# Performance work log

Hardware: AMD Instinct MI355X
Metric: run time of the kernel (lower is better)

Reference implementation:

```python
import jax, jax.numpy as jnp
import numpy as np

C = 512
CI = C // 4  # inter_channels
EPS = 1e-5


def _conv1x1(x, w, b):
    # x: [B,C,H,W], w: [O,C], b: [O] -> [B,O,H,W]
    return jnp.einsum('bchw,oc->bohw', x, w) + b[None, :, None, None]


def _maxpool2(t):
    # 2x2 max pool, stride 2 (NCHW)
    b, c, h, w = t.shape
    return t.reshape(b, c, h // 2, 2, w // 2, 2).max(axis=(3, 5))


def setup_inputs() -> dict:
    key = jax.random.key(0)
    ks = jax.random.split(key, 9)
    B, H, W = 8, 64, 64
    s_in = 1.0 / np.sqrt(C)
    s_ci = 1.0 / np.sqrt(CI)
    return {
        'x': jax.random.normal(ks[0], (B, C, H, W), jnp.float32),
        'g_w': jax.random.normal(ks[1], (CI, C), jnp.float32) * s_in,
        'g_b': jnp.zeros((CI,), jnp.float32),
        'phi_w': jax.random.normal(ks[2], (CI, C), jnp.float32) * s_in,
        'phi_b': jnp.zeros((CI,), jnp.float32),
        'theta_w': jax.random.normal(ks[3], (CI, C), jnp.float32) * s_in,
        'theta_b': jnp.zeros((CI,), jnp.float32),
        'W_w': jax.random.normal(ks[4], (C, CI), jnp.float32) * s_ci,
        'W_b': jnp.zeros((C,), jnp.float32),
        'ln_gamma': jax.random.normal(ks[5], (C,), jnp.float32) * 0.02 + 1.0,
        'ln_beta': jnp.zeros((C,), jnp.float32),
    }


def reference(x, g_w, g_b, phi_w, phi_b, theta_w, theta_b, W_w, W_b, ln_gamma, ln_beta):
    B, Cc, H, Wd = x.shape
    N = H * Wd
    # projections; g and phi are maxpool-downsampled (N/4 key/value positions)
    g_x = _maxpool2(_conv1x1(x, g_w, g_b)).reshape(B, CI, N // 4)          # [B,Ci,M]
    phi_x = _maxpool2(_conv1x1(x, phi_w, phi_b)).reshape(B, CI, N // 4)    # [B,Ci,M]
    theta_x = _conv1x1(x, theta_w, theta_b).reshape(B, CI, N)              # [B,Ci,N]
    # attention: QK^T -> softmax -> V
    f = jnp.einsum('bcn,bcm->bnm', theta_x, phi_x)                          # [B,N,M]
    attn = jax.nn.softmax(f, axis=-1)
    y = jnp.einsum('bnm,bcm->bcn', attn, g_x).reshape(B, CI, H, Wd)         # [B,Ci,H,W]
    # output projection + channels-first LayerNorm + residual
    W_y = _conv1x1(y, W_w, W_b)                                             # [B,C,H,W]
    mu = W_y.mean(axis=1, keepdims=True)
    var = W_y.var(axis=1, keepdims=True)
    W_y = (W_y - mu) * jax.lax.rsqrt(var + EPS)
    W_y = W_y * ln_gamma[None, :, None, None] + ln_beta[None, :, None, None]
    return W_y + x
```

## Files before the change

### kernel.cpp

```cpp
#include <hip/hip_runtime.h>
#include <math.h>

constexpr int Cc  = 512;
constexpr int CIc = 128;
constexpr int Bc  = 8;
constexpr int Nc  = 4096;
constexpr int Mc  = 1024;

typedef __bf16 bf16x8 __attribute__((ext_vector_type(8)));
typedef float  f32x4  __attribute__((ext_vector_type(4)));

__device__ __forceinline__ unsigned short f2bf(float f) {
  unsigned u = __float_as_uint(f);
  u += 0x7fffu + ((u >> 16) & 1u);
  return (unsigned short)(u >> 16);
}
__device__ __forceinline__ float bf2f(unsigned short h) {
  return __uint_as_float((unsigned)h << 16);
}
__device__ __forceinline__ unsigned pack2bf(float lo, float hi) {
  return (unsigned)f2bf(lo) | ((unsigned)f2bf(hi) << 16);
}

__device__ __forceinline__ void gload16(const void* g, void* lds) {
  __builtin_amdgcn_global_load_lds(
      (const __attribute__((address_space(1))) unsigned int*)g,
      (__attribute__((address_space(3))) unsigned int*)lds, 16, 0, 0);
}

__global__ __launch_bounds__(256) void k_prep(
    const float* __restrict__ gw, const float* __restrict__ pw,
    const float* __restrict__ tw, const float* __restrict__ Ww,
    const float* __restrict__ gb, const float* __restrict__ pb,
    const float* __restrict__ tb,
    unsigned short* __restrict__ wcat, unsigned short* __restrict__ wwb,
    float* __restrict__ bcat) {
  constexpr float L2E = 1.4426950408889634f;
  int i = blockIdx.x * 256 + threadIdx.x;
  if (i < 49152) {
    int c = i >> 7, q = i & 127;
    const float* src = (c < 128) ? tw + (size_t)c * 512
                     : (c < 256) ? pw + (size_t)(c - 128) * 512
                                 : gw + (size_t)(c - 256) * 512;
    float sc = (c < 128) ? L2E : 1.f;
    float4 v = *(const float4*)(src + q * 4);
    ushort4 o;
    o.x = f2bf(v.x * sc); o.y = f2bf(v.y * sc);
    o.z = f2bf(v.z * sc); o.w = f2bf(v.w * sc);
    *(ushort4*)(wcat + (size_t)c * 512 + q * 4) = o;
  } else if (i < 65536) {
    int i2 = i - 49152;
    int c = i2 >> 5, q = i2 & 31;
    float4 v = *(const float4*)(Ww + (size_t)c * 128 + q * 4);
    ushort4 o;
    o.x = f2bf(v.x); o.y = f2bf(v.y); o.z = f2bf(v.z); o.w = f2bf(v.w);
    *(ushort4*)(wwb + (size_t)c * 128 + q * 4) = o;
  } else if (i < 65920) {
    int j = i - 65536;
    bcat[j] = (j < 128) ? tb[j] * L2E : (j < 256) ? pb[j - 128] : gb[j - 256];
  }
}

__global__ __launch_bounds__(512) void k_conv_all(
    const float* __restrict__ x, const unsigned short* __restrict__ wcat,
    const float* __restrict__ bcat,
    unsigned short* __restrict__ theta_t, unsigned short* __restrict__ phi_t,
    unsigned short* __restrict__ gbuf) {
  __shared__ __align__(16) char smem[147456];
  const int b = blockIdx.y, h2 = blockIdx.x, n0 = h2 * 128;
  const int t = threadIdx.x;
  const int w = t >> 6, l = t & 63, lr = l & 15, lg = l >> 4;

  const char* wsrc = (const char*)wcat;
  int woff[6];
#pragma unroll
  for (int i = 0; i < 6; ++i) {
    int r = (w * 6 + i) * 8 + (l >> 3);
    woff[i] = r * 1024 + (((l & 7) * 16) ^ ((r & 7) << 4));
  }

  const float* xb = x + (size_t)b * Cc * Nc + n0 + w * 16 + lr;

  float xraw0[16], xraw1[16];
#define LOADX(dst_, k0_)                                                  \
  {                                                                       \
    _Pragma("unroll")                                                     \
    for (int ks = 0; ks < 2; ++ks)                                        \
      _Pragma("unroll")                                                   \
      for (int j = 0; j < 8; ++j)                                         \
        dst_[ks * 8 + j] = xb[(size_t)((k0_) + ks * 32 + lg * 8 + j) * Nc]; \
  }
#define STAGEW(buf_, k0_)                                                 \
  {                                                                       \
    char* dst_ = smem + (buf_) * 49152;                                   \
    _Pragma("unroll")                                                     \
    for (int i = 0; i < 6; ++i)                                           \
      gload16(wsrc + (size_t)(k0_) * 2 + woff[i], dst_ + (w * 6 + i) * 1024); \
  }
#define CONVERT(src_)                                                     \
  {                                                                       \
    _Pragma("unroll")                                                     \
    for (int ks = 0; ks < 2; ++ks) {                                      \
      union { unsigned u[4]; bf16x8 v; } ab;                              \
      _Pragma("unroll")                                                   \
      for (int q = 0; q < 4; ++q)                                         \
        ab.u[q] = pack2bf(src_[ks * 8 + 2 * q], src_[ks * 8 + 2 * q + 1]); \
      af[ks] = ab.v;                                                      \
    }                                                                     \
  }

  f32x4 acc[24];
#pragma unroll
  for (int tc = 0; tc < 24; ++tc) acc[tc] = (f32x4){0.f, 0.f, 0.f, 0.f};

  STAGEW(0, 0);
  LOADX(xraw0, 0);
  STAGEW(1, 64);
  LOADX(xraw1, 64);
  asm volatile("s_waitcnt vmcnt(22)" ::: "memory");
  __builtin_amdgcn_s_barrier();

#pragma unroll
  for (int c = 0; c < 8; ++c) {
    bf16x8 af[2];
    if ((c & 1) == 0) {
      CONVERT(xraw0);
      if (c < 6) { STAGEW((c + 2) % 3, (c + 2) * 64); LOADX(xraw0, (c + 2) * 64); }
    } else {
      CONVERT(xraw1);
      if (c < 6) { STAGEW((c + 2) % 3, (c + 2) * 64); LOADX(xraw1, (c + 2) * 64); }
    }
    const char* Wb = smem + (c % 3) * 49152;
    __builtin_amdgcn_s_setprio(1);
#pragma unroll
    for (int ks = 0; ks < 2; ++ks)
#pragma unroll
      for (int tc = 0; tc < 24; ++tc) {
        int r = tc * 16 + lr;
        bf16x8 bfr = *(const bf16x8*)(
            Wb + r * 128 + ((lg * 16 + ks * 64) ^ ((lr & 7) << 4)));
        acc[tc] = __builtin_amdgcn_mfma_f32_16x16x32_bf16(af[ks], bfr, acc[tc], 0, 0, 0);
      }
    __builtin_amdgcn_s_setprio(0);
    if (c < 6) {
      asm volatile("s_waitcnt vmcnt(22)" ::: "memory");
      __builtin_amdgcn_s_barrier();
    } else if (c == 6) {
      asm volatile("s_waitcnt vmcnt(16)" ::: "memory");
      __builtin_amdgcn_s_barrier();
    }
  }
#undef LOADX
#undef STAGEW
#undef CONVERT

  __syncthreads();
  unsigned short* PG = (unsigned short*)smem;
  unsigned short* Yt = (unsigned short*)(smem + 67584);
  const int rbase = w * 16 + lg * 4;

#pragma unroll
  for (int tc = 8; tc < 24; ++tc) {
    float bv = bcat[tc * 16 + lr];
#pragma unroll
    for (int reg = 0; reg < 4; ++reg)
      PG[(rbase + reg) * 264 + tc * 16 + lr - 128] = f2bf(acc[tc][reg] + bv);
  }
  if (w < 4) {
#pragma unroll
    for (int tc = 0; tc < 8; ++tc) {
      float bv = bcat[tc * 16 + lr];
#pragma unroll
      for (int reg = 0; reg < 4; ++reg)
        Yt[(rbase + reg) * 136 + tc * 16 + lr] = f2bf(acc[tc][reg] + bv);
    }
  }
  __syncthreads();
#pragma unroll
  for (int it = 0; it < 2; ++it) {
    int idx = it * 512 + t, n = idx >> 4, j = idx & 15;
    *(bf16x8*)(theta_t + (((size_t)(b * Nc + n0 + n)) << 7) + j * 8) =
        *(const bf16x8*)(Yt + n * 136 + j * 8);
  }
  {
    int mloc = t >> 4, j = t & 15;
    const unsigned short* r0 = &PG[(2 * mloc) * 264 + j * 8];
    const unsigned short* r1 = &PG[(2 * mloc + 1) * 264 + j * 8];
    const unsigned short* r2 = &PG[(64 + 2 * mloc) * 264 + j * 8];
    const unsigned short* r3 = &PG[(65 + 2 * mloc) * 264 + j * 8];
    unsigned short o[8];
#pragma unroll
    for (int q = 0; q < 8; ++q)
      o[q] = f2bf(fmaxf(fmaxf(bf2f(r0[q]), bf2f(r1[q])),
                        fmaxf(bf2f(r2[q]), bf2f(r3[q]))));
    unsigned short* dp = phi_t + (((size_t)(b * Mc + h2 * 32 + mloc)) << 7) + j * 8;
    *(ushort4*)dp = *(ushort4*)o;
    *(ushort4*)(dp + 4) = *(ushort4*)(o + 4);
  }
  {
    int ci = t >> 2, mq = t & 3;
    unsigned short tmp[8];
#pragma unroll
    for (int q = 0; q < 8; ++q) {
      int w2 = mq * 8 + q;
      float m0 = fmaxf(
          fmaxf(bf2f(PG[(2 * w2) * 264 + 128 + ci]),
                bf2f(PG[(2 * w2 + 1) * 264 + 128 + ci])),
          fmaxf(bf2f(PG[(64 + 2 * w2) * 264 + 128 + ci]),
                bf2f(PG[(65 + 2 * w2) * 264 + 128 + ci])));
      tmp[q] = f2bf(m0);
    }
    unsigned short* dst = gbuf + ((size_t)(b * CIc + ci)) * Mc + h2 * 32 + mq * 8;
    *(ushort4*)(dst) = *(ushort4*)(tmp);
    *(ushort4*)(dst + 4) = *(ushort4*)(tmp + 4);
  }
  __syncthreads();
  if (w >= 4) {
#pragma unroll
    for (int tc = 0; tc < 8; ++tc) {
      float bv = bcat[tc * 16 + lr];
#pragma unroll
      for (int reg = 0; reg < 4; ++reg)
        Yt[((w - 4) * 16 + lg * 4 + reg) * 136 + tc * 16 + lr] =
            f2bf(acc[tc][reg] + bv);
    }
  }
  __syncthreads();
#pragma unroll
  for (int it = 0; it < 2; ++it) {
    int idx = it * 512 + t, n = idx >> 4, j = idx & 15;
    *(bf16x8*)(theta_t + (((size_t)(b * Nc + n0 + 64 + n)) << 7) + j * 8) =
        *(const bf16x8*)(Yt + n * 136 + j * 8);
  }
}

__global__ __launch_bounds__(256) void k_attn_mfma(
    const unsigned short* __restrict__ theta_t,
    const unsigned short* __restrict__ phi_t,
    const unsigned short* __restrict__ gv,
    unsigned short* __restrict__ y_t) {
  __shared__ __align__(16) char Kb[2][16384];
  __shared__ __align__(16) char Vb[2][16384];
  __shared__ __align__(16) unsigned Psd[4][16][36];
  const int b = blockIdx.y, n0 = blockIdx.x * 64;
  const int tid = threadIdx.x;
  const int w = tid >> 6, l = tid & 63;
  const int lr = l & 15, lg = l >> 4;

  const int krow_l = l >> 4, kchunk = (l & 15) * 16;
  const int vrow_l = l >> 3, vchunk = (l & 7) * 16;
  int koff[4], voff[4];
#pragma unroll
  for (int i = 0; i < 4; ++i) {
    int kr = w * 16 + i * 4 + krow_l;
    koff[i] = kr * 256 + (kchunk ^ ((kr & 7) << 4));
    int vr = w * 32 + i * 8 + vrow_l;
    voff[i] = vr * 2048 + (vchunk ^ ((vr & 7) << 4));
  }
  const char* kbase = (const char*)(phi_t + (((size_t)(b * Mc)) << 7));
  const char* vbase = (const char*)(gv + (((size_t)b) << 17));

  auto stage = [&](int buf, int t) {
#pragma unroll
    for (int i = 0; i < 4; ++i)
      gload16(kbase + t * 16384 + koff[i], &Kb[buf][(w * 4 + i) * 1024]);
#pragma unroll
    for (int i = 0; i < 4; ++i)
      gload16(vbase + t * 128 + voff[i], &Vb[buf][(w * 4 + i) * 1024]);
  };

  bf16x8 qf[4];
  {
    const unsigned short* qp =
        theta_t + (((size_t)(b * Nc + n0 + w * 16 + lr)) << 7);
#pragma unroll
    for (int kk = 0; kk < 4; ++kk)
      qf[kk] = *(const bf16x8*)(qp + kk * 32 + lg * 8);
  }
  f32x4 of[8];
#pragma unroll
  for (int ct = 0; ct < 8; ++ct) of[ct] = (f32x4){0.f, 0.f, 0.f, 0.f};
  float run_m = -1e30f, run_l = 0.f;

  stage(0, 0);
  asm volatile("s_waitcnt vmcnt(0)" ::: "memory");
  __builtin_amdgcn_s_barrier();

  for (int t = 0; t < Mc / 64; ++t) {
    const int cur = t & 1;
    if (t + 1 < Mc / 64) stage(cur ^ 1, t + 1);
    const char* Ks = Kb[cur];
    const char* Vs = Vb[cur];
    f32x4 sm[4];
    __builtin_amdgcn_s_setprio(1);
#pragma unroll
    for (int mt = 0; mt < 4; ++mt) {
      f32x4 s = (f32x4){0.f, 0.f, 0.f, 0.f};
#pragma unroll
      for (int kk = 0; kk < 4; ++kk) {
        bf16x8 kf = *(const bf16x8*)(
            Ks + (mt * 16 + lr) * 256 + ((kk * 64 + lg * 16) ^ ((lr & 7) << 4)));
        s = __builtin_amdgcn_mfma_f32_16x16x32_bf16(kf, qf[kk], s, 0, 0, 0);
      }
      sm[mt] = s;
    }
    __builtin_amdgcn_s_setprio(0);
    float mx;
    {
      float m0 = fmaxf(fmaxf(sm[0][0], sm[0][1]), fmaxf(sm[0][2], sm[0][3]));
      float m1 = fmaxf(fmaxf(sm[1][0], sm[1][1]), fmaxf(sm[1][2], sm[1][3]));
      float m2 = fmaxf(fmaxf(sm[2][0], sm[2][1]), fmaxf(sm[2][2], sm[2][3]));
      float m3 = fmaxf(fmaxf(sm[3][0], sm[3][1]), fmaxf(sm[3][2], sm[3][3]));
      mx = fmaxf(fmaxf(m0, m1), fmaxf(m2, m3));
      mx = fmaxf(mx, __shfl_xor(mx, 16));
      mx = fmaxf(mx, __shfl_xor(mx, 32));
    }
    if (__any(mx > run_m + 8.f)) {
      float nm = fmaxf(run_m, mx);
      float sc = __builtin_amdgcn_exp2f(run_m - nm);
      run_m = nm;
      run_l *= sc;
#pragma unroll
      for (int reg = 0; reg < 4; ++reg) {
        float scr = __shfl(sc, lg * 20 + reg);
#pragma unroll
        for (int ct = 0; ct < 8; ++ct) of[ct][reg] *= scr;
      }
    }
    unsigned pk[4][2];
    float rowsum = 0.f;
#pragma unroll
    for (int mt = 0; mt < 4; ++mt) {
      float p0 = __builtin_amdgcn_exp2f(sm[mt][0] - run_m);
      float p1 = __builtin_amdgcn_exp2f(sm[mt][1] - run_m);
      float p2 = __builtin_amdgcn_exp2f(sm[mt][2] - run_m);
      float p3 = __builtin_amdgcn_exp2f(sm[mt][3] - run_m);
      rowsum += (p0 + p1) + (p2 + p3);
      asm("v_cvt_pk_bf16_f32 %0, %1, %2" : "=v"(pk[mt][0]) : "v"(p0), "v"(p1));
      asm("v_cvt_pk_bf16_f32 %0, %1, %2" : "=v"(pk[mt][1]) : "v"(p2), "v"(p3));
    }
    rowsum += __shfl_xor(rowsum, 16);
    rowsum += __shfl_xor(rowsum, 32);
    run_l += rowsum;
#pragma unroll
    for (int mt = 0; mt < 4; ++mt) {
      Psd[w][lr][8 * mt + 2 * lg + 0] = pk[mt][0];
      Psd[w][lr][8 * mt + 2 * lg + 1] = pk[mt][1];
    }
    bf16x8 pa0 = *(const bf16x8*)&Psd[w][lr][lg * 4];
    bf16x8 pa1 = *(const bf16x8*)&Psd[w][lr][16 + lg * 4];
    __builtin_amdgcn_s_setprio(1);
#pragma unroll
    for (int ct = 0; ct < 8; ++ct) {
      bf16x8 vf0 = *(const bf16x8*)(
          Vs + (ct * 16 + lr) * 128 + ((lg * 16) ^ ((lr & 7) << 4)));
      of[ct] = __builtin_amdgcn_mfma_f32_16x16x32_bf16(pa0, vf0, of[ct], 0, 0, 0);
      bf16x8 vf1 = *(const bf16x8*)(
          Vs + (ct * 16 + lr) * 128 + ((64 + lg * 16) ^ ((lr & 7) << 4)));
      of[ct] = __builtin_amdgcn_mfma_f32_16x16x32_bf16(pa1, vf1, of[ct], 0, 0, 0);
    }
    __builtin_amdgcn_s_setprio(0);
    asm volatile("s_waitcnt vmcnt(0)" ::: "memory");
    __builtin_amdgcn_s_barrier();
  }
  float invl = 1.f / run_l;
  float invr[4];
#pragma unroll
  for (int reg = 0; reg < 4; ++reg) invr[reg] = __shfl(invl, lg * 20 + reg);
  unsigned short* Ys = (unsigned short*)Kb;
#pragma unroll
  for (int ct = 0; ct < 8; ++ct)
#pragma unroll
    for (int reg = 0; reg < 4; ++reg)
      Ys[(w * 16 + lg * 4 + reg) * 128 + ct * 16 + lr] =
          f2bf(of[ct][reg] * invr[reg]);
  __syncthreads();
#pragma unroll
  for (int it = 0; it < 4; ++it) {
    int i = it * 256 + tid;
    int r = i >> 4, cl = i & 15;
    *(bf16x8*)(y_t + (((size_t)(b * Nc + n0 + r)) << 7) + cl * 8) =
        *(const bf16x8*)(Ys + r * 128 + cl * 8);
  }
}

__global__ __launch_bounds__(256) void k_wconv_mfma(
    const unsigned short* __restrict__ y_t, const unsigned short* __restrict__ wwb,
    const float* __restrict__ wbias, const float* __restrict__ gamma,
    const float* __restrict__ beta, const float* __restrict__ x,
    float* __restrict__ out) {
  __shared__ __align__(16) char smem[65536];
  float* Ys = (float*)smem;
  const int b = blockIdx.y, n0 = blockIdx.x * 64;
  const int t = threadIdx.x;
  const int w = t >> 6, l = t & 63, lr = l & 15, lg = l >> 4;

  int woff[8];
#pragma unroll
  for (int i = 0; i < 8; ++i) {
    int r = (w * 8 + i) * 4 + (l >> 4);
    woff[i] = r * 256 + ((((l & 15) * 16)) ^ ((r & 7) << 4));
  }
  const char* wbase = (const char*)wwb;

  auto stageW = [&](int buf, int cc) {
#pragma unroll
    for (int i = 0; i < 8; ++i)
      gload16(wbase + cc * 32768 + woff[i],
              smem + buf * 32768 + (w * 8 + i) * 1024);
  };

  bf16x8 qf[4];
  {
    const unsigned short* qp = y_t + (((size_t)(b * Nc + n0 + w * 16 + lr)) << 7);
#pragma unroll
    for (int kk = 0; kk < 4; ++kk)
      qf[kk] = *(const bf16x8*)(qp + kk * 32 + lg * 8);
  }
  f32x4 acc[32];
#pragma unroll
  for (int i = 0; i < 32; ++i) acc[i] = (f32x4){0.f, 0.f, 0.f, 0.f};

  stageW(0, 0);
  asm volatile("s_waitcnt vmcnt(0)" ::: "memory");
  __builtin_amdgcn_s_barrier();

#pragma unroll
  for (int cc = 0; cc < 4; ++cc) {
    const int cur = cc & 1;
    if (cc < 3) stageW(cur ^ 1, cc + 1);
    const char* WTs = smem + cur * 32768;
    __builtin_amdgcn_s_setprio(1);
#pragma unroll
    for (int tc = 0; tc < 8; ++tc) {
      f32x4 a = acc[cc * 8 + tc];
      int r = tc * 16 + lr;
#pragma unroll
      for (int kk = 0; kk < 4; ++kk) {
        bf16x8 kf = *(const bf16x8*)(
            WTs + r * 256 + ((kk * 64 + lg * 16) ^ ((lr & 7) << 4)));
        a = __builtin_amdgcn_mfma_f32_16x16x32_bf16(qf[kk], kf, a, 0, 0, 0);
      }
      acc[cc * 8 + tc] = a;
    }
    __builtin_amdgcn_s_setprio(0);
    asm volatile("s_waitcnt vmcnt(0)" ::: "memory");
    __builtin_amdgcn_s_barrier();
  }

  float s[4] = {0.f, 0.f, 0.f, 0.f}, q[4] = {0.f, 0.f, 0.f, 0.f};
#pragma unroll
  for (int cc = 0; cc < 4; ++cc)
#pragma unroll
    for (int tc = 0; tc < 8; ++tc) {
      float wb = wbias[cc * 128 + tc * 16 + lr];
      f32x4 a = acc[cc * 8 + tc];
#pragma unroll
      for (int reg = 0; reg < 4; ++reg) {
        a[reg] += wb;
        s[reg] += a[reg];
        q[reg] += a[reg] * a[reg];
      }
      acc[cc * 8 + tc] = a;
    }
  float mu[4], rs[4];
#pragma unroll
  for (int reg = 0; reg < 4; ++reg) {
    float sv = s[reg], qv = q[reg];
    sv += __shfl_xor(sv, 1); qv += __shfl_xor(qv, 1);
    sv += __shfl_xor(sv, 2); qv += __shfl_xor(qv, 2);
    sv += __shfl_xor(sv, 4); qv += __shfl_xor(qv, 4);
    sv += __shfl_xor(sv, 8); qv += __shfl_xor(qv, 8);
    mu[reg] = sv * (1.f / 512.f);
    float var = qv * (1.f / 512.f) - mu[reg] * mu[reg];
    rs[reg] = rsqrtf(var + 1e-5f);
  }
#pragma unroll
  for (int cc = 0; cc < 4; ++cc) {
    __syncthreads();
#pragma unroll
    for (int tc = 0; tc < 8; ++tc) {
      int c = cc * 128 + tc * 16 + lr;
      float ga = gamma[c], be = beta[c];
#pragma unroll
      for (int reg = 0; reg < 4; ++reg)
        Ys[(tc * 16 + lr) * 72 + w * 16 + lg * 4 + reg] =
            (acc[cc * 8 + tc][reg] - mu[reg]) * rs[reg] * ga + be;
    }
    __syncthreads();
#pragma unroll
    for (int it = 0; it < 8; ++it) {
      int idx = it * 256 + t;
      int r = idx >> 4, j = idx & 15;
      float4 v = *(const float4*)&Ys[r * 72 + j * 4];
      size_t gaddr = ((size_t)b * Cc + cc * 128 + r) * Nc + n0 + j * 4;
      float4 xv = *(const float4*)&x[gaddr];
      float4 o;
      o.x = v.x + xv.x; o.y = v.y + xv.y; o.z = v.z + xv.z; o.w = v.w + xv.w;
      *(float4*)&out[gaddr] = o;
    }
  }
}

extern "C" void kernel_launch(void* const* d_in, const int* in_sizes, int n_in,
                              void* d_out, int out_size, void* d_ws, size_t ws_size,
                              hipStream_t stream) {
  const float* x       = (const float*)d_in[0];
  const float* g_w     = (const float*)d_in[1];
  const float* g_b     = (const float*)d_in[2];
  const float* phi_w   = (const float*)d_in[3];
  const float* phi_b   = (const float*)d_in[4];
  const float* theta_w = (const float*)d_in[5];
  const float* theta_b = (const float*)d_in[6];
  const float* W_w     = (const float*)d_in[7];
  const float* W_b     = (const float*)d_in[8];
  const float* ln_g    = (const float*)d_in[9];
  const float* ln_b    = (const float*)d_in[10];
  float* out = (float*)d_out;

  unsigned short* theta_t = (unsigned short*)d_ws;
  unsigned short* y_t     = theta_t + (size_t)Bc * Nc * CIc;
  unsigned short* phi_t   = y_t + (size_t)Bc * Nc * CIc;
  unsigned short* gbuf    = phi_t + (size_t)Bc * Mc * CIc;
  unsigned short* wcat    = gbuf + (size_t)Bc * Mc * CIc;
  unsigned short* wwb     = wcat + (size_t)384 * 512;
  float*          bcat    = (float*)(wwb + (size_t)512 * 128);

  k_prep<<<dim3(258), dim3(256), 0, stream>>>(
      g_w, phi_w, theta_w, W_w, g_b, phi_b, theta_b, wcat, wwb, bcat);
  k_conv_all<<<dim3(Nc / 128, Bc), dim3(512), 0, stream>>>(
      x, wcat, bcat, theta_t, phi_t, gbuf);
  k_attn_mfma<<<dim3(Nc / 64, Bc), dim3(256), 0, stream>>>(
      theta_t, phi_t, gbuf, y_t);
  k_wconv_mfma<<<dim3(Nc / 64, Bc), dim3(256), 0, stream>>>(
      y_t, wwb, W_b, ln_g, ln_b, x, out);
}
```

Before: 100.2 us.

## Software-pipeline attention loop: overlap next tile QK^T with current softmax and PV

Restructures the flash-attention main loop into a two-stage software pipeline. Each step computes QK^T for the next key tile while softmax and PV run on the current one, and K and V loads are staged separately so K is prefetched one tile further ahead. The aim is to hide the latency of the softmax's dependent scalar work behind MFMA work and to overlap loads better. The cost is a second score register set (higher register pressure) and more complex barrier placement, plus an extra sync before the output write.

```diff
diff --git a/kernel.cpp b/kernel.cpp
--- a/kernel.cpp
+++ b/kernel.cpp
@@ -260,10 +260,12 @@
   const char* kbase = (const char*)(phi_t + (((size_t)(b * Mc)) << 7));
   const char* vbase = (const char*)(gv + (((size_t)b) << 17));
 
-  auto stage = [&](int buf, int t) {
+  auto stageK = [&](int buf, int t) {
 #pragma unroll
     for (int i = 0; i < 4; ++i)
       gload16(kbase + t * 16384 + koff[i], &Kb[buf][(w * 4 + i) * 1024]);
+  };
+  auto stageV = [&](int buf, int t) {
 #pragma unroll
     for (int i = 0; i < 4; ++i)
       gload16(vbase + t * 128 + voff[i], &Vb[buf][(w * 4 + i) * 1024]);
@@ -281,93 +283,116 @@
 #pragma unroll
   for (int ct = 0; ct < 8; ++ct) of[ct] = (f32x4){0.f, 0.f, 0.f, 0.f};
   float run_m = -1e30f, run_l = 0.f;
-
-  stage(0, 0);
+  f32x4 smA[4], smB[4];
+
+#define QKSTEP(SM, KSP)                                                    \
+  {                                                                        \
+    __builtin_amdgcn_s_setprio(1);                                         \
+    _Pragma("unroll") for (int mt = 0; mt < 4; ++mt) {                     \
+      f32x4 s_ = (f32x4){0.f, 0.f, 0.f, 0.f};                              \
+      _Pragma("unroll") for (int kk = 0; kk < 4; ++kk) {                   \
+        bf16x8 kf = *(const bf16x8*)((KSP) + (mt * 16 + lr) * 256 +        \
+            ((kk * 64 + lg * 16) ^ ((lr & 7) << 4)));                      \
+        s_ = __builtin_amdgcn_mfma_f32_16x16x32_bf16(kf, qf[kk], s_, 0, 0, 0); \
+      }                                                                    \
+      SM[mt] = s_;                                                         \
+    }                                                                      \
+    __builtin_amdgcn_s_setprio(0);                                         \
+  }
+
+#define SOFTMAX(SM)                                                        \
+  {                                                                        \
+    float mx;                                                              \
+    {                                                                      \
+      float m0 = fmaxf(fmaxf(SM[0][0], SM[0][1]), fmaxf(SM[0][2], SM[0][3])); \
+      float m1 = fmaxf(fmaxf(SM[1][0], SM[1][1]), fmaxf(SM[1][2], SM[1][3])); \
+      float m2 = fmaxf(fmaxf(SM[2][0], SM[2][1]), fmaxf(SM[2][2], SM[2][3])); \
+      float m3 = fmaxf(fmaxf(SM[3][0], SM[3][1]), fmaxf(SM[3][2], SM[3][3])); \
+      mx = fmaxf(fmaxf(m0, m1), fmaxf(m2, m3));                            \
+      mx = fmaxf(mx, __shfl_xor(mx, 16));                                  \
+      mx = fmaxf(mx, __shfl_xor(mx, 32));                                  \
+    }                                                                      \
+    if (__any(mx > run_m + 8.f)) {                                         \
+      float nm = fmaxf(run_m, mx);                                         \
+      float sc = __builtin_amdgcn_exp2f(run_m - nm);                       \
+      run_m = nm;                                                          \
+      run_l *= sc;                                                         \
+      _Pragma("unroll") for (int reg = 0; reg < 4; ++reg) {                \
+        float scr = __shfl(sc, lg * 20 + reg);                             \
+        _Pragma("unroll") for (int ct = 0; ct < 8; ++ct) of[ct][reg] *= scr; \
+      }                                                                    \
+    }                                                                      \
+    float rowsum = 0.f;                                                    \
+    _Pragma("unroll") for (int mt = 0; mt < 4; ++mt) {                     \
+      float p0 = __builtin_amdgcn_exp2f(SM[mt][0] - run_m);                \
+      float p1 = __builtin_amdgcn_exp2f(SM[mt][1] - run_m);                \
+      float p2 = __builtin_amdgcn_exp2f(SM[mt][2] - run_m);                \
+      float p3 = __builtin_amdgcn_exp2f(SM[mt][3] - run_m);                \
+      rowsum += (p0 + p1) + (p2 + p3);                                     \
+      unsigned pk01, pk23;                                                 \
+      asm("v_cvt_pk_bf16_f32 %0, %1, %2" : "=v"(pk01) : "v"(p0), "v"(p1)); \
+      asm("v_cvt_pk_bf16_f32 %0, %1, %2" : "=v"(pk23) : "v"(p2), "v"(p3)); \
+      Psd[w][lr][8 * mt + 2 * lg + 0] = pk01;                              \
+      Psd[w][lr][8 * mt + 2 * lg + 1] = pk23;                              \
+    }                                                                      \
+    rowsum += __shfl_xor(rowsum, 16);                                      \
+    rowsum += __shfl_xor(rowsum, 32);                                      \
+    run_l += rowsum;                                                       \
+  }
+
+#define PVSTEP(VSP)                                                        \
+  {                                                                        \
+    bf16x8 pa0 = *(const bf16x8*)&Psd[w][lr][lg * 4];                      \
+    bf16x8 pa1 = *(const bf16x8*)&Psd[w][lr][16 + lg * 4];                 \
+    __builtin_amdgcn_s_setprio(1);                                         \
+    _Pragma("unroll") for (int ct = 0; ct < 8; ++ct) {                     \
+      bf16x8 vf0 = *(const bf16x8*)((VSP) + (ct * 16 + lr) * 128 +         \
+          ((lg * 16) ^ ((lr & 7) << 4)));                                  \
+      of[ct] = __builtin_amdgcn_mfma_f32_16x16x32_bf16(pa0, vf0, of[ct], 0, 0, 0); \
+      bf16x8 vf1 = *(const bf16x8*)((VSP) + (ct * 16 + lr) * 128 +         \
+          ((64 + lg * 16) ^ ((lr & 7) << 4)));                             \
+      of[ct] = __builtin_amdgcn_mfma_f32_16x16x32_bf16(pa1, vf1, of[ct], 0, 0, 0); \
+    }                                                                      \
+    __builtin_amdgcn_s_setprio(0);                                         \
+  }
+
+  stageK(0, 0);
+  stageK(1, 1);
+  stageV(0, 0);
   asm volatile("s_waitcnt vmcnt(0)" ::: "memory");
   __builtin_amdgcn_s_barrier();
-
-  for (int t = 0; t < Mc / 64; ++t) {
-    const int cur = t & 1;
-    if (t + 1 < Mc / 64) stage(cur ^ 1, t + 1);
-    const char* Ks = Kb[cur];
-    const char* Vs = Vb[cur];
-    f32x4 sm[4];
-    __builtin_amdgcn_s_setprio(1);
-#pragma unroll
-    for (int mt = 0; mt < 4; ++mt) {
-      f32x4 s = (f32x4){0.f, 0.f, 0.f, 0.f};
-#pragma unroll
-      for (int kk = 0; kk < 4; ++kk) {
-        bf16x8 kf = *(const bf16x8*)(
-            Ks + (mt * 16 + lr) * 256 + ((kk * 64 + lg * 16) ^ ((lr & 7) << 4)));
-        s = __builtin_amdgcn_mfma_f32_16x16x32_bf16(kf, qf[kk], s, 0, 0, 0);
-      }
-      sm[mt] = s;
-    }
-    __builtin_amdgcn_s_setprio(0);
-    float mx;
-    {
-      float m0 = fmaxf(fmaxf(sm[0][0], sm[0][1]), fmaxf(sm[0][2], sm[0][3]));
-      float m1 = fmaxf(fmaxf(sm[1][0], sm[1][1]), fmaxf(sm[1][2], sm[1][3]));
-      float m2 = fmaxf(fmaxf(sm[2][0], sm[2][1]), fmaxf(sm[2][2], sm[2][3]));
-      float m3 = fmaxf(fmaxf(sm[3][0], sm[3][1]), fmaxf(sm[3][2], sm[3][3]));
-      mx = fmaxf(fmaxf(m0, m1), fmaxf(m2, m3));
-      mx = fmaxf(mx, __shfl_xor(mx, 16));
-      mx = fmaxf(mx, __shfl_xor(mx, 32));
-    }
-    if (__any(mx > run_m + 8.f)) {
-      float nm = fmaxf(run_m, mx);
-      float sc = __builtin_amdgcn_exp2f(run_m - nm);
-      run_m = nm;
-      run_l *= sc;
-#pragma unroll
-      for (int reg = 0; reg < 4; ++reg) {
-        float scr = __shfl(sc, lg * 20 + reg);
-#pragma unroll
-        for (int ct = 0; ct < 8; ++ct) of[ct][reg] *= scr;
-      }
-    }
-    unsigned pk[4][2];
-    float rowsum = 0.f;
-#pragma unroll
-    for (int mt = 0; mt < 4; ++mt) {
-      float p0 = __builtin_amdgcn_exp2f(sm[mt][0] - run_m);
-      float p1 = __builtin_amdgcn_exp2f(sm[mt][1] - run_m);
-      float p2 = __builtin_amdgcn_exp2f(sm[mt][2] - run_m);
-      float p3 = __builtin_amdgcn_exp2f(sm[mt][3] - run_m);
-      rowsum += (p0 + p1) + (p2 + p3);
-      asm("v_cvt_pk_bf16_f32 %0, %1, %2" : "=v"(pk[mt][0]) : "v"(p0), "v"(p1));
-      asm("v_cvt_pk_bf16_f32 %0, %1, %2" : "=v"(pk[mt][1]) : "v"(p2), "v"(p3));
-    }
-    rowsum += __shfl_xor(rowsum, 16);
-    rowsum += __shfl_xor(rowsum, 32);
-    run_l += rowsum;
-#pragma unroll
-    for (int mt = 0; mt < 4; ++mt) {
-      Psd[w][lr][8 * mt + 2 * lg + 0] = pk[mt][0];
-      Psd[w][lr][8 * mt + 2 * lg + 1] = pk[mt][1];
-    }
-    bf16x8 pa0 = *(const bf16x8*)&Psd[w][lr][lg * 4];
-    bf16x8 pa1 = *(const bf16x8*)&Psd[w][lr][16 + lg * 4];
-    __builtin_amdgcn_s_setprio(1);
-#pragma unroll
-    for (int ct = 0; ct < 8; ++ct) {
-      bf16x8 vf0 = *(const bf16x8*)(
-          Vs + (ct * 16 + lr) * 128 + ((lg * 16) ^ ((lr & 7) << 4)));
-      of[ct] = __builtin_amdgcn_mfma_f32_16x16x32_bf16(pa0, vf0, of[ct], 0, 0, 0);
-      bf16x8 vf1 = *(const bf16x8*)(
-          Vs + (ct * 16 + lr) * 128 + ((64 + lg * 16) ^ ((lr & 7) << 4)));
-      of[ct] = __builtin_amdgcn_mfma_f32_16x16x32_bf16(pa1, vf1, of[ct], 0, 0, 0);
-    }
-    __builtin_amdgcn_s_setprio(0);
+  QKSTEP(smA, (const char*)Kb[0]);
+  __builtin_amdgcn_s_barrier();
+
+  for (int tp = 0; tp < 8; ++tp) {
+    const int t0 = tp * 2;
+    if (t0 + 2 < 16) stageK(0, t0 + 2);
+    { const char* ksn = (const char*)Kb[1]; QKSTEP(smB, ksn); }
+    stageV(1, t0 + 1);
+    SOFTMAX(smA);
+    PVSTEP((const char*)Vb[0]);
     asm volatile("s_waitcnt vmcnt(0)" ::: "memory");
     __builtin_amdgcn_s_barrier();
-  }
+    if (t0 + 3 < 16) stageK(1, t0 + 3);
+    if (t0 + 2 < 16) { const char* ksn = (const char*)Kb[0]; QKSTEP(smA, ksn); }
+    if (t0 + 2 < 16) stageV(0, t0 + 2);
+    SOFTMAX(smB);
+    PVSTEP((const char*)Vb[1]);
+    if (t0 + 2 < 16) {
+      asm volatile("s_waitcnt vmcnt(0)" ::: "memory");
+      __builtin_amdgcn_s_barrier();
+    }
+  }
+#undef QKSTEP
+#undef SOFTMAX
+#undef PVSTEP
+
   float invl = 1.f / run_l;
   float invr[4];
 #pragma unroll
   for (int reg = 0; reg < 4; ++reg) invr[reg] = __shfl(invl, lg * 20 + reg);
   unsigned short* Ys = (unsigned short*)Kb;
+  __syncthreads();
 #pragma unroll
   for (int ct = 0; ct < 8; ++ct)
 #pragma unroll
```

Result: no change. 100.4 us (+0.2%).
